# Performance work log

Measured on AMD Instinct MI355X. Metric: run time of the kernel, lower is better.

Reference implementation:

```python
import jax, jax.numpy as jnp
import numpy as np

G, N, E, F, D = 4096, 64, 256, 64, 128
H1, H2 = 16, 2
EP = 32768
EPS = 1e-15
MAX_LOGSTD = 10.0


def setup_inputs() -> dict:
    key = jax.random.key(0)
    ks = jax.random.split(key, 16)
    def lin(k, i, o):
        return (jax.random.normal(k, (i, o), jnp.float32) / np.sqrt(i)).astype(jnp.float32)
    inp = {}
    inp["x"] = jax.random.normal(ks[0], (G, N, F), jnp.float32)
    inp["edge_index"] = jax.random.randint(ks[1], (G, 2, E), 0, N, dtype=jnp.int32)
    inp["edge_weight"] = jax.random.uniform(ks[2], (G, E), jnp.float32)
    inp["pos_edges"] = jax.random.randint(ks[3], (2, EP), 0, G, dtype=jnp.int32)
    inp["neg_edges"] = jax.random.randint(ks[4], (2, EP), 0, G, dtype=jnp.int32)
    inp["eps"] = jax.random.normal(ks[5], (G, D), jnp.float32)
    inp["W_gcn1"] = lin(ks[6], F, D); inp["b_gcn1"] = jnp.zeros((D,), jnp.float32)
    inp["W_fc1"] = lin(ks[7], D, H1); inp["b_fc1"] = jnp.zeros((H1,), jnp.float32)
    inp["W_fc2"] = lin(ks[8], H1, H2); inp["b_fc2"] = jnp.zeros((H2,), jnp.float32)
    inp["W_c1"] = lin(ks[9], D, 2 * D); inp["b_c1"] = jnp.zeros((2 * D,), jnp.float32)
    inp["W_mu"] = lin(ks[10], 2 * D, D); inp["b_mu"] = jnp.zeros((D,), jnp.float32)
    inp["W_ls"] = lin(ks[11], 2 * D, D); inp["b_ls"] = jnp.zeros((D,), jnp.float32)
    inp["emb"] = jax.random.normal(ks[12], (G, D), jnp.float32)
    inp["W_lin1"] = lin(ks[13], 2 * D, 2 * D); inp["b_lin1"] = jnp.zeros((2 * D,), jnp.float32)
    inp["W_lin2"] = lin(ks[14], 2 * D, 2 * D); inp["b_lin2"] = jnp.zeros((2 * D,), jnp.float32)
    return inp


def gcn_conv(x, src, dst, w, W, b, n):
    # PyG GCNConv: add self-loops (weight 1), sym-normalize, aggregate at target (col).
    xw = x @ W                                      # [n, out]
    deg = jnp.zeros((n,), xw.dtype).at[dst].add(w) + 1.0
    dinv = jax.lax.rsqrt(deg)
    norm = dinv[src] * w * dinv[dst]
    agg = jnp.zeros_like(xw).at[dst].add(xw[src] * norm[:, None])
    agg = agg + xw * (dinv * dinv)[:, None]         # self-loop term
    return agg + b


def sage_graph(x, ei, w, W_gcn1, b_gcn1, W_fc1, b_fc1, W_fc2, b_fc2):
    src, dst = ei[0], ei[1]
    h = gcn_conv(x, src, dst, w, W_gcn1, b_gcn1, N)          # [N, D]
    a1 = jnp.tanh(h @ W_fc1 + b_fc1)                         # [N, H1]
    S = jax.nn.softmax(a1 @ W_fc2 + b_fc2, axis=1)           # [N, 2]
    # get_laplacian(normalization='sym'): L = I - D^{-1/2} A D^{-1/2}, deg from row
    deg = jnp.zeros((N,), x.dtype).at[src].add(w)
    dinv = jnp.where(deg > 0, jax.lax.rsqrt(jnp.maximum(deg, 1e-30)), 0.0)
    lw = -dinv[src] * w * dinv[dst]
    L = jnp.zeros((N, N), x.dtype).at[src, dst].add(lw) + jnp.eye(N, dtype=x.dtype)
    new_adj = S.T @ (L @ S)                                  # [2, 2]
    norm_adj = new_adj / jnp.maximum(jnp.sum(jnp.abs(new_adj), axis=1, keepdims=True), 1e-12)
    diag = jnp.diagonal(norm_adj)
    pos_penalty = jnp.mean((diag - 1.0) ** 2)                # MSE vs ones(2)
    g_emb = jnp.mean(S.T @ h, axis=0)                        # [D]
    return g_emb, pos_penalty


def gcn_conv_unw(x, src, dst, W, b, n):
    return gcn_conv(x, src, dst, jnp.ones(src.shape, x.dtype), W, b, n)


def reference(x, edge_index, edge_weight, pos_edges, neg_edges, eps,
              W_gcn1, b_gcn1, W_fc1, b_fc1, W_fc2, b_fc2,
              W_c1, b_c1, W_mu, b_mu, W_ls, b_ls, emb,
              W_lin1, b_lin1, W_lin2, b_lin2):
    g_embs, pens = jax.vmap(sage_graph,
                            in_axes=(0, 0, 0, None, None, None, None, None, None))(
        x, edge_index, edge_weight, W_gcn1, b_gcn1, W_fc1, b_fc1, W_fc2, b_fc2)
    positive_penalty = jnp.mean(pens)
    # VGAE encode over graph-level graph (dropout in eval mode = identity)
    ps, pd = pos_edges[0], pos_edges[1]
    h = jax.nn.relu(gcn_conv_unw(g_embs, ps, pd, W_c1, b_c1, G))
    mu = gcn_conv_unw(h, ps, pd, W_mu, b_mu, G)
    logstd = jnp.minimum(gcn_conv_unw(h, ps, pd, W_ls, b_ls, G), MAX_LOGSTD)
    z = mu + eps * jnp.exp(logstd)                            # reparametrize
    zc = jnp.concatenate([emb, z], axis=-1)                   # [G, 2D]
    def pred(ei):
        fx = zc[ei[0]] @ W_lin1 + b_lin1
        fy = zc[ei[1]] @ W_lin2 + b_lin2
        return jax.nn.sigmoid(jnp.sum(fx * fy, axis=1))
    pos_pred = pred(pos_edges)
    neg_pred = pred(neg_edges)
    rec_loss = -jnp.mean(jnp.log(pos_pred + EPS)) - jnp.mean(jnp.log(1.0 - neg_pred + EPS))
    kl = -0.5 * jnp.mean(jnp.sum(1.0 + 2.0 * logstd - mu ** 2 - jnp.exp(2.0 * logstd), axis=1))
    pre_loss = rec_loss + kl / G
    return pre_loss, positive_penalty, pos_pred, neg_pred
```

## Files before the change

### kernel.cpp

```cpp
#include <hip/hip_runtime.h>
#include <hip/hip_bf16.h>
#include <math.h>

#define GG   4096
#define NNODE 64
#define EEDGE 256
#define FFEAT 64
#define DDIM 128
#define EP   32768

__device__ __forceinline__ float fast_tanh(float x) {
    float e = __expf(2.0f * x);
    return 1.0f - 2.0f / (e + 1.0f);
}

__global__ void k_prep(const float* __restrict__ Wg, const float* __restrict__ Wf1,
                       const float* __restrict__ bf1, const float* __restrict__ bg,
                       float* __restrict__ Wgf1, float* __restrict__ bcomb,
                       float* __restrict__ bg32, int* __restrict__ icnt_g) {
    int t = threadIdx.x;
    for (int o = t; o < 1024; o += 256) {
        int r = o >> 4, j = o & 15;
        int kk = r >> 2, q = r & 3;
        int f = q * 16 + kk;
        float s = 0.f;
        for (int d = 0; d < 128; ++d) s += Wg[f * 128 + d] * Wf1[d * 16 + j];
        Wgf1[o] = s;
    }
    if (t < 16) {
        float s = bf1[t];
        for (int d = 0; d < 128; ++d) s += bg[d] * Wf1[d * 16 + t];
        bcomb[t] = s;
    }
    if (t >= 128) bg32[t - 128] = 32.0f * bg[t - 128];
    for (int i = t; i < 4096; i += 256) icnt_g[i] = 0;
}

__global__ __launch_bounds__(256) void k_pg(
    const float* __restrict__ x, const int* __restrict__ ei, const float* __restrict__ ew,
    const float* __restrict__ Wgf1, const float* __restrict__ bcomb,
    const float* __restrict__ Wf2, const float* __restrict__ bf2,
    float* __restrict__ Qh, float* __restrict__ pens)
{
    __shared__ __align__(16) float sm[6656];
    float* xs    = sm;
    float* Wp    = sm + 4352;
    int*   lsrc  = (int*)(sm + 5376);
    float* lnrm  = sm + 5632;
    int*   icnt  = (int*)(sm + 5888);
    int*   offs  = (int*)(sm + 5952);
    int*   curs  = (int*)(sm + 6016);
    float* degw  = sm + 6080;
    float* dinvs = sm + 6144;
    float* deg2s = sm + 6208;
    float* dinv2s= sm + 6272;
    float* Ss    = sm + 6336;
    float* LSs   = sm + 6464;
    float* bcs   = sm + 6592;
    float* Wf2s  = sm + 6608;
    float* bf2s  = sm + 6640;

    const int g = blockIdx.x;
    const int t = threadIdx.x;
    const float* xg = x + (size_t)g * 4096;

    int es, ed; float wv;
    {
        const int* eg = ei + (size_t)g * 512;
        es = eg[t];
        ed = eg[256 + t];
        wv = ew[(size_t)g * 256 + t];
        for (int i = t; i < 1024; i += 256) {
            int n = i >> 4, k = (i & 15) * 4;
            *(float4*)&xs[n * 68 + k] = *(const float4*)&xg[n * 64 + k];
        }
        *(float4*)&Wp[t * 4] = *(const float4*)&Wgf1[t * 4];
        if (t < 16) bcs[t] = bcomb[t];
        if (t < 32) Wf2s[t] = Wf2[t];
        if (t < 2)  bf2s[t] = bf2[t];
        if (t < 64) { icnt[t] = 0; degw[t] = 1.0f; deg2s[t] = 0.0f; }
        if (t < 128) LSs[t] = 0.0f;
    }
    __syncthreads();

    atomicAdd(&icnt[ed], 1);
    atomicAdd(&degw[ed], wv);
    atomicAdd(&deg2s[es], wv);
    __syncthreads();

    if (t < 64) {
        int v = icnt[t], own = v;
        for (int o = 1; o < 64; o <<= 1) { int u = __shfl_up(v, o); if (t >= o) v += u; }
        int excl = v - own;
        offs[t] = excl; curs[t] = excl;
        dinvs[t] = rsqrtf(degw[t]);
        float dg = deg2s[t];
        dinv2s[t] = dg > 0.0f ? rsqrtf(fmaxf(dg, 1e-30f)) : 0.0f;
    }
    __syncthreads();

    float lw;
    {
        int pos = atomicAdd(&curs[ed], 1);
        lsrc[pos] = es;
        lnrm[pos] = dinvs[es] * wv * dinvs[ed];
        lw = -dinv2s[es] * wv * dinv2s[ed];
    }
    __syncthreads();

    const int n = t >> 2, q = t & 3, base = q * 16;
    float Av[16];
    {
        float sc = dinvs[n] * dinvs[n];
        const float* xrow = &xs[n * 68 + base];
        *(float4*)&Av[0]  = *(const float4*)&xrow[0];
        *(float4*)&Av[4]  = *(const float4*)&xrow[4];
        *(float4*)&Av[8]  = *(const float4*)&xrow[8];
        *(float4*)&Av[12] = *(const float4*)&xrow[12];
#pragma unroll
        for (int kk = 0; kk < 16; ++kk) Av[kk] *= sc;
        int o = offs[n], c = icnt[n];
        for (int j = 0; j < c; ++j) {
            int s = lsrc[o + j];
            float nm = lnrm[o + j];
            const float* xr = &xs[s * 68 + base];
            float4 X0 = *(const float4*)&xr[0];
            float4 X1 = *(const float4*)&xr[4];
            float4 X2 = *(const float4*)&xr[8];
            float4 X3 = *(const float4*)&xr[12];
            Av[0]  += X0.x * nm; Av[1]  += X0.y * nm; Av[2]  += X0.z * nm; Av[3]  += X0.w * nm;
            Av[4]  += X1.x * nm; Av[5]  += X1.y * nm; Av[6]  += X1.z * nm; Av[7]  += X1.w * nm;
            Av[8]  += X2.x * nm; Av[9]  += X2.y * nm; Av[10] += X2.z * nm; Av[11] += X2.w * nm;
            Av[12] += X3.x * nm; Av[13] += X3.y * nm; Av[14] += X3.z * nm; Av[15] += X3.w * nm;
        }
        __syncthreads();
        float* xw = &xs[n * 68 + base];
        *(float4*)&xw[0]  = *(float4*)&Av[0];
        *(float4*)&xw[4]  = *(float4*)&Av[4];
        *(float4*)&xw[8]  = *(float4*)&Av[8];
        *(float4*)&xw[12] = *(float4*)&Av[12];
    }
    __syncthreads();

    {
        float pj[16];
#pragma unroll
        for (int j = 0; j < 16; ++j) pj[j] = 0.f;
#pragma unroll
        for (int kk = 0; kk < 16; ++kk) {
            float a = Av[kk];
            const float* wr = &Wp[((kk << 2) + q) << 4];
            float4 w0 = *(const float4*)&wr[0];
            float4 w1 = *(const float4*)&wr[4];
            float4 w2 = *(const float4*)&wr[8];
            float4 w3 = *(const float4*)&wr[12];
            pj[0]  += a * w0.x; pj[1]  += a * w0.y; pj[2]  += a * w0.z; pj[3]  += a * w0.w;
            pj[4]  += a * w1.x; pj[5]  += a * w1.y; pj[6]  += a * w1.z; pj[7]  += a * w1.w;
            pj[8]  += a * w2.x; pj[9]  += a * w2.y; pj[10] += a * w2.z; pj[11] += a * w2.w;
            pj[12] += a * w3.x; pj[13] += a * w3.y; pj[14] += a * w3.z; pj[15] += a * w3.w;
        }
#pragma unroll
        for (int j = 0; j < 16; ++j) {
            pj[j] += __shfl_xor(pj[j], 1);
            pj[j] += __shfl_xor(pj[j], 2);
        }
        float z0 = bf2s[0], z1 = bf2s[1];
#pragma unroll
        for (int j = 0; j < 16; ++j) {
            float aj = fast_tanh(pj[j] + bcs[j]);
            z0 += aj * Wf2s[2 * j];
            z1 += aj * Wf2s[2 * j + 1];
        }
        float m = fmaxf(z0, z1);
        float e0 = __expf(z0 - m), e1 = __expf(z1 - m);
        float inv = 1.0f / (e0 + e1);
        if (q == 0) { Ss[n * 2] = e0 * inv; Ss[n * 2 + 1] = e1 * inv; }
    }
    __syncthreads();

    {
        float s0 = Ss[ed * 2], s1 = Ss[ed * 2 + 1];
        atomicAdd(&LSs[es * 2],     lw * s0);
        atomicAdd(&LSs[es * 2 + 1], lw * s1);
    }
    __syncthreads();

    if (t < 64) {
        float s0 = Ss[t * 2], s1 = Ss[t * 2 + 1];
        float l0 = s0 + LSs[t * 2], l1 = s1 + LSs[t * 2 + 1];
        float p00 = s0 * l0, p01 = s0 * l1, p10 = s1 * l0, p11 = s1 * l1;
        for (int o = 32; o; o >>= 1) {
            p00 += __shfl_down(p00, o); p01 += __shfl_down(p01, o);
            p10 += __shfl_down(p10, o); p11 += __shfl_down(p11, o);
        }
        if (t == 0) {
            float r0 = fmaxf(fabsf(p00) + fabsf(p01), 1e-12f);
            float r1 = fmaxf(fabsf(p10) + fabsf(p11), 1e-12f);
            float d0 = p00 / r0 - 1.0f, d1 = p11 / r1 - 1.0f;
            pens[g] = 0.5f * (d0 * d0 + d1 * d1);
        }
    }
    {
        int k = t & 63, p = t >> 6;
        float qk = 0.f;
#pragma unroll 4
        for (int nn = 0; nn < 16; ++nn)
            qk += xs[(p * 16 + nn) * 68 + k];
        Wp[p * 64 + k] = qk;
    }
    __syncthreads();
    if (t < 64)
        Qh[(size_t)g * 64 + t] = 0.5f * (Wp[t] + Wp[64 + t] + Wp[128 + t] + Wp[192 + t]);
}

__global__ void k_cnt(const int* __restrict__ pd, int* __restrict__ icnt) {
    int e = blockIdx.x * 256 + threadIdx.x;
    atomicAdd(&icnt[pd[e]], 1);
}

__global__ void k_scan(const int* __restrict__ icnt, int* __restrict__ offs,
                       int* __restrict__ curs, float* __restrict__ dinv) {
    __shared__ int wsum[4];
    int t = threadIdx.x;
    int base = t * 16;
    int l0,l1,l2,l3,l4,l5,l6,l7,l8,l9,l10,l11,l12,l13,l14,l15;
    l0=icnt[base+0]; l1=icnt[base+1]; l2=icnt[base+2]; l3=icnt[base+3];
    l4=icnt[base+4]; l5=icnt[base+5]; l6=icnt[base+6]; l7=icnt[base+7];
    l8=icnt[base+8]; l9=icnt[base+9]; l10=icnt[base+10]; l11=icnt[base+11];
    l12=icnt[base+12]; l13=icnt[base+13]; l14=icnt[base+14]; l15=icnt[base+15];
    int s = l0+l1+l2+l3+l4+l5+l6+l7+l8+l9+l10+l11+l12+l13+l14+l15;
    int lane = t & 63, w = t >> 6;
    int v = s;
    for (int o = 1; o < 64; o <<= 1) { int u = __shfl_up(v, o); if (lane >= o) v += u; }
    if (lane == 63) wsum[w] = v;
    __syncthreads();
    int woff = 0;
    for (int i = 0; i < 4; ++i) if (i < w) woff += wsum[i];
    int run = woff + v - s;
#define SC(L, I) offs[base+(I)] = run; curs[base+(I)] = run; \
    dinv[base+(I)] = rsqrtf((float)(L) + 1.0f); run += L;
    SC(l0,0) SC(l1,1) SC(l2,2) SC(l3,3) SC(l4,4) SC(l5,5) SC(l6,6) SC(l7,7)
    SC(l8,8) SC(l9,9) SC(l10,10) SC(l11,11) SC(l12,12) SC(l13,13) SC(l14,14) SC(l15,15)
#undef SC
}

__global__ void k_place(const int* __restrict__ pe, const float* __restrict__ dinv,
                        int* __restrict__ curs, int* __restrict__ csr_src,
                        float* __restrict__ csr_nrm) {
    int e = blockIdx.x * 256 + threadIdx.x;
    int s = pe[e], d = pe[EP + e];
    int pos = atomicAdd(&curs[d], 1);
    csr_src[pos] = s;
    csr_nrm[pos] = dinv[s] * dinv[d];
}

__global__ void k_gather128(const int* __restrict__ offs, const int* __restrict__ icnt,
                            const int* __restrict__ csr_src, const float* __restrict__ csr_nrm,
                            const float* __restrict__ dinv, const float* __restrict__ in,
                            float* __restrict__ out) {
    int g = blockIdx.x, d = threadIdx.x;
    float dv = dinv[g];
    float acc = in[(size_t)g * 128 + d] * dv * dv;
    int o = offs[g], c = icnt[g];
    for (int j = 0; j < c; ++j)
        acc += in[(size_t)csr_src[o + j] * 128 + d] * csr_nrm[o + j];
    out[(size_t)g * 128 + d] = acc;
}

__global__ void k_gather256(const int* __restrict__ offs, const int* __restrict__ icnt,
                            const int* __restrict__ csr_src, const float* __restrict__ csr_nrm,
                            const float* __restrict__ dinv, const float* __restrict__ in,
                            float* __restrict__ out) {
    int g = blockIdx.x, d = threadIdx.x;
    float dv = dinv[g];
    float acc = in[(size_t)g * 256 + d] * dv * dv;
    int o = offs[g], c = icnt[g];
    for (int j = 0; j < c; ++j)
        acc += in[(size_t)csr_src[o + j] * 256 + d] * csr_nrm[o + j];
    out[(size_t)g * 256 + d] = acc;
}

__global__ __launch_bounds__(256) void k_gemm(
    const float* __restrict__ A,
    const float* __restrict__ B0, const float* __restrict__ bias0, float* __restrict__ C0,
    const float* __restrict__ B1, const float* __restrict__ bias1, float* __restrict__ C1,
    int M, int K, int N, int dorelu)
{
    __shared__ __align__(16) float lds[2 * 4352];
    const float* B = B0; const float* bias = bias0; float* C = C0;
    int by = blockIdx.y;
    if (B1 != nullptr && by >= (int)(gridDim.y >> 1)) {
        B = B1; bias = bias1; C = C1; by -= (gridDim.y >> 1);
    }
    const int mb = blockIdx.x * 64, nbb = by * 64;
    const int t = threadIdx.x;
    const int tm4 = (t >> 4) * 4, tn4 = (t & 15) * 4;
    const int ma = t >> 2, ka = (t & 3) * 8;
    const int kb = t >> 3, nb8 = (t & 7) * 8;

    float4 pa0, pa1, pb0, pb1;
#define LOADT(K0) { \
    const float* Ap = &A[(size_t)(mb + ma) * K + (K0) + ka]; \
    pa0 = *(const float4*)Ap; pa1 = *(const float4*)(Ap + 4); \
    const float* Bp = &B[(size_t)((K0) + kb) * N + nbb + nb8]; \
    pb0 = *(const float4*)Bp; pb1 = *(const float4*)(Bp + 4); }
#define STORET(BUF) { \
    float* At_ = lds + (BUF) * 4352; \
    At_[(ka + 0) * 68 + ma] = pa0.x; At_[(ka + 1) * 68 + ma] = pa0.y; \
    At_[(ka + 2) * 68 + ma] = pa0.z; At_[(ka + 3) * 68 + ma] = pa0.w; \
    At_[(ka + 4) * 68 + ma] = pa1.x; At_[(ka + 5) * 68 + ma] = pa1.y; \
    At_[(ka + 6) * 68 + ma] = pa1.z; At_[(ka + 7) * 68 + ma] = pa1.w; \
    float* Bs_ = lds + (BUF) * 4352 + 2176; \
    *(float4*)&Bs_[kb * 68 + nb8] = pb0; *(float4*)&Bs_[kb * 68 + nb8 + 4] = pb1; }

    float4 ca0 = {0,0,0,0}, ca1 = {0,0,0,0}, ca2 = {0,0,0,0}, ca3 = {0,0,0,0};
    const int nk0 = K >> 5;
    LOADT(0)
    STORET(0)
    __syncthreads();
    for (int it = 0; it < nk0; ++it) {
        if (it + 1 < nk0) LOADT((it + 1) * 32)
        const float* At_ = lds + (it & 1) * 4352;
        const float* Bs_ = At_ + 2176;
#pragma unroll
        for (int k = 0; k < 32; ++k) {
            float4 av = *(const float4*)&At_[k * 68 + tm4];
            float4 bv = *(const float4*)&Bs_[k * 68 + tn4];
            ca0.x += av.x * bv.x; ca0.y += av.x * bv.y; ca0.z += av.x * bv.z; ca0.w += av.x * bv.w;
            ca1.x += av.y * bv.x; ca1.y += av.y * bv.y; ca1.z += av.y * bv.z; ca1.w += av.y * bv.w;
            ca2.x += av.z * bv.x; ca2.y += av.z * bv.y; ca2.z += av.z * bv.z; ca2.w += av.z * bv.w;
            ca3.x += av.w * bv.x; ca3.y += av.w * bv.y; ca3.z += av.w * bv.z; ca3.w += av.w * bv.w;
        }
        if (it + 1 < nk0) {
            STORET((it + 1) & 1)
            __syncthreads();
        }
    }
#undef LOADT
#undef STORET
    float4 bv4 = {0, 0, 0, 0};
    if (bias) bv4 = *(const float4*)&bias[nbb + tn4];
#define CST(I, CV) { \
    float4 v; v.x = CV.x + bv4.x; v.y = CV.y + bv4.y; v.z = CV.z + bv4.z; v.w = CV.w + bv4.w; \
    if (dorelu) { v.x = fmaxf(v.x, 0.f); v.y = fmaxf(v.y, 0.f); v.z = fmaxf(v.z, 0.f); v.w = fmaxf(v.w, 0.f); } \
    *(float4*)&C[(size_t)(mb + tm4 + (I)) * N + nbb + tn4] = v; }
    CST(0, ca0) CST(1, ca1) CST(2, ca2) CST(3, ca3)
#undef CST
}

__global__ void k_fin_z(const float* __restrict__ mu_arr, const float* __restrict__ ls_arr,
                        const float* __restrict__ eps, const float* __restrict__ emb,
                        float* __restrict__ zc, float* __restrict__ klp) {
    __shared__ float smw[2];
    int g = blockIdx.x, d = threadIdx.x;
    int idx = g * 128 + d;
    float mu = mu_arr[idx];
    float ls = fminf(ls_arr[idx], 10.0f);
    float e  = __expf(ls);
    float z = mu + eps[idx] * e;
    zc[(size_t)g * 256 + d] = emb[idx];
    zc[(size_t)g * 256 + 128 + d] = z;
    float term = 1.0f + 2.0f * ls - mu * mu - e * e;
    for (int o = 32; o; o >>= 1) term += __shfl_down(term, o);
    if ((d & 63) == 0) smw[d >> 6] = term;
    __syncthreads();
    if (d == 0) klp[g] = smw[0] + smw[1];
}

__global__ void k_pred(const float* __restrict__ A, const float* __restrict__ B,
                       const int* __restrict__ pos, const int* __restrict__ neg,
                       float* __restrict__ out, float* __restrict__ predp) {
    __shared__ float smw[16];
    int t = threadIdx.x, sub = t >> 4, l = t & 15;
    int eg = blockIdx.x * 16 + sub;
    int isneg = eg >= EP;
    int e = eg - (isneg ? EP : 0);
    const int* eix = isneg ? neg : pos;
    int s = eix[e], d = eix[EP + e];
    const float4* Ar = (const float4*)(A + (size_t)s * 256);
    const float4* Br = (const float4*)(B + (size_t)d * 256);
    float dot = 0.f;
#pragma unroll
    for (int q = 0; q < 4; ++q) {
        float4 av = Ar[l + 16 * q], bv = Br[l + 16 * q];
        dot += av.x * bv.x + av.y * bv.y + av.z * bv.z + av.w * bv.w;
    }
    for (int o = 8; o; o >>= 1) dot += __shfl_down(dot, o);
    if (l == 0) {
        float p = 1.0f / (1.0f + __expf(-dot));
        float term;
        if (isneg) { out[2 + EP + e] = p; term = __logf(1.0f - p + 1e-15f); }
        else       { out[2 + e] = p;      term = __logf(p + 1e-15f); }
        smw[sub] = term;
    }
    __syncthreads();
    if (t == 0) {
        float s16 = 0.f;
#pragma unroll
        for (int i = 0; i < 16; ++i) s16 += smw[i];
        predp[blockIdx.x] = s16;
    }
}

__global__ void k_final(const float* __restrict__ pens, const float* __restrict__ klp,
                        const float* __restrict__ predp, float* __restrict__ out) {
    __shared__ float sm[16];
    int t = threadIdx.x;
    float s_pen = 0.f, s_kl = 0.f, s_pos = 0.f, s_neg = 0.f;
    for (int i = t; i < 4096; i += 256) { s_pen += pens[i]; s_kl += klp[i]; }
    for (int i = t; i < 2048; i += 256) { s_pos += predp[i]; s_neg += predp[2048 + i]; }
    for (int o = 32; o; o >>= 1) {
        s_pen += __shfl_down(s_pen, o); s_kl += __shfl_down(s_kl, o);
        s_pos += __shfl_down(s_pos, o); s_neg += __shfl_down(s_neg, o);
    }
    int w = t >> 6;
    if ((t & 63) == 0) { sm[w] = s_pen; sm[4 + w] = s_kl; sm[8 + w] = s_pos; sm[12 + w] = s_neg; }
    __syncthreads();
    if (t == 0) {
        float pen = sm[0] + sm[1] + sm[2] + sm[3];
        float kls = sm[4] + sm[5] + sm[6] + sm[7];
        float pos = sm[8] + sm[9] + sm[10] + sm[11];
        float neg = sm[12] + sm[13] + sm[14] + sm[15];
        float rec = -(pos / 32768.0f) - (neg / 32768.0f);
        out[0] = rec - 0.5f * kls / (4096.0f * 4096.0f);
        out[1] = pen * (1.0f / 4096.0f);
    }
}

extern "C" void kernel_launch(void* const* d_in, const int* in_sizes, int n_in,
                              void* d_out, int out_size, void* d_ws, size_t ws_size,
                              hipStream_t stream) {
    const float* x   = (const float*)d_in[0];
    const int*   ei  = (const int*)d_in[1];
    const float* ew  = (const float*)d_in[2];
    const int*   pos = (const int*)d_in[3];
    const int*   neg = (const int*)d_in[4];
    const float* eps = (const float*)d_in[5];
    const float* Wg  = (const float*)d_in[6];
    const float* bg  = (const float*)d_in[7];
    const float* Wf1 = (const float*)d_in[8];
    const float* bf1 = (const float*)d_in[9];
    const float* Wf2 = (const float*)d_in[10];
    const float* bf2 = (const float*)d_in[11];
    const float* Wc1 = (const float*)d_in[12];
    const float* bc1 = (const float*)d_in[13];
    const float* Wmu = (const float*)d_in[14];
    const float* bmu = (const float*)d_in[15];
    const float* Wls = (const float*)d_in[16];
    const float* bls = (const float*)d_in[17];
    const float* emb = (const float*)d_in[18];
    const float* Wl1 = (const float*)d_in[19];
    const float* bl1 = (const float*)d_in[20];
    const float* Wl2 = (const float*)d_in[21];
    const float* bl2 = (const float*)d_in[22];
    float* out = (float*)d_out;
    float* ws  = (float*)d_ws;

    float* g_embs  = ws + 0;
    float* dinv    = ws + 524288;
    int*   icnt_g  = (int*)(ws + 528384);
    int*   off_g   = (int*)(ws + 532480);
    int*   cur_g   = (int*)(ws + 536576);
    int*   csr_src = (int*)(ws + 540672);
    float* csr_nrm = ws + 573440;
    float* Qh      = ws + 606208;
    float* ga      = ws + 868352;
    float* h       = ws + 1392640;
    float* ha      = ws + 2441216;
    float* mu_arr  = ws + 3489792;
    float* ls_arr  = ws + 4014080;
    float* zc      = ws + 4538368;
    float* Abuf    = ws + 5586944;
    float* Bbuf    = ws + 6635520;
    float* pens    = ws + 7684096;
    float* klp     = ws + 7688192;
    float* predp   = ws + 7692288;
    float* Wgf1    = ws + 7708672;
    float* bcomb   = ws + 7709696;
    float* bg32    = ws + 7709712;

    k_prep<<<1, 256, 0, stream>>>(Wg, Wf1, bf1, bg, Wgf1, bcomb, bg32, icnt_g);
    k_pg<<<GG, 256, 0, stream>>>(x, ei, ew, Wgf1, bcomb, Wf2, bf2, Qh, pens);
    k_gemm<<<dim3(64, 2), 256, 0, stream>>>(Qh, Wg, bg32, g_embs,
                                            nullptr, nullptr, nullptr, GG, 64, 128, 0);

    k_cnt<<<EP / 256, 256, 0, stream>>>(pos + EP, icnt_g);
    k_scan<<<1, 256, 0, stream>>>(icnt_g, off_g, cur_g, dinv);
    k_place<<<EP / 256, 256, 0, stream>>>(pos, dinv, cur_g, csr_src, csr_nrm);

    k_gather128<<<GG, 128, 0, stream>>>(off_g, icnt_g, csr_src, csr_nrm, dinv, g_embs, ga);
    k_gemm<<<dim3(64, 4), 256, 0, stream>>>(ga, Wc1, bc1, h,
                                            nullptr, nullptr, nullptr, GG, 128, 256, 1);

    k_gather256<<<GG, 256, 0, stream>>>(off_g, icnt_g, csr_src, csr_nrm, dinv, h, ha);
    k_gemm<<<dim3(64, 4), 256, 0, stream>>>(ha, Wmu, bmu, mu_arr,
                                            Wls, bls, ls_arr, GG, 256, 128, 0);
    k_fin_z<<<GG, 128, 0, stream>>>(mu_arr, ls_arr, eps, emb, zc, klp);

    k_gemm<<<dim3(64, 8), 256, 0, stream>>>(zc, Wl1, bl1, Abuf,
                                            Wl2, bl2, Bbuf, GG, 256, 256, 0);

    k_pred<<<(2 * EP) / 16, 256, 0, stream>>>(Abuf, Bbuf, pos, neg, out, predp);
    k_final<<<1, 256, 0, stream>>>(pens, klp, predp, out);
}
```

Before: 320.8 us.

## Project node features before aggregation and compute pooled readout via column weights

Adds a separate kernel that multiplies all node features by the fused GCN-FC1 weight first, so per-graph aggregation works on 16-wide projected rows instead of 64-wide raw features. The per-graph kernel now uses much less shared memory. It computes the pooled readout Qh as a weighted sum of x rows, using per-node column sums of the normalization accumulated with atomics. The cost is an extra launch and a round trip of the projected features through global memory, plus re-reading x from global in the readout.

After: 337.9 us. 5.3% more time.

```diff
diff --git a/kernel.cpp b/kernel.cpp
--- a/kernel.cpp
+++ b/kernel.cpp
@@ -20,9 +20,7 @@
                        float* __restrict__ bg32, int* __restrict__ icnt_g) {
     int t = threadIdx.x;
     for (int o = t; o < 1024; o += 256) {
-        int r = o >> 4, j = o & 15;
-        int kk = r >> 2, q = r & 3;
-        int f = q * 16 + kk;
+        int f = o >> 4, j = o & 15;
         float s = 0.f;
         for (int d = 0; d < 128; ++d) s += Wg[f * 128 + d] * Wf1[d * 16 + j];
         Wgf1[o] = s;
@@ -36,33 +34,69 @@
     for (int i = t; i < 4096; i += 256) icnt_g[i] = 0;
 }
 
+__global__ __launch_bounds__(256) void k_y(
+    const float* __restrict__ x, const float* __restrict__ W,
+    float* __restrict__ Y)
+{
+    __shared__ __align__(16) float Ws[1024];
+    const int t = threadIdx.x;
+    *(float4*)&Ws[t * 4] = *(const float4*)&W[t * 4];
+    const int rr = t >> 2, q = t & 3;
+    const size_t r0 = (size_t)blockIdx.x * 256 + rr;
+    const float* x0 = &x[r0 * 64];
+    __syncthreads();
+    float4 p0 = {0,0,0,0}, p1 = {0,0,0,0}, p2 = {0,0,0,0}, p3 = {0,0,0,0};
+#pragma unroll 4
+    for (int kb = 0; kb < 16; ++kb) {
+        float4 xv0 = *(const float4*)&x0[kb * 4];
+        float4 xv1 = *(const float4*)&x0[4096 + kb * 4];
+        float4 xv2 = *(const float4*)&x0[8192 + kb * 4];
+        float4 xv3 = *(const float4*)&x0[12288 + kb * 4];
+#pragma unroll
+        for (int kk = 0; kk < 4; ++kk) {
+            float4 wv = *(const float4*)&Ws[(kb * 4 + kk) * 16 + q * 4];
+            float a0 = (&xv0.x)[kk], a1 = (&xv1.x)[kk];
+            float a2 = (&xv2.x)[kk], a3 = (&xv3.x)[kk];
+            p0.x += a0 * wv.x; p0.y += a0 * wv.y; p0.z += a0 * wv.z; p0.w += a0 * wv.w;
+            p1.x += a1 * wv.x; p1.y += a1 * wv.y; p1.z += a1 * wv.z; p1.w += a1 * wv.w;
+            p2.x += a2 * wv.x; p2.y += a2 * wv.y; p2.z += a2 * wv.z; p2.w += a2 * wv.w;
+            p3.x += a3 * wv.x; p3.y += a3 * wv.y; p3.z += a3 * wv.z; p3.w += a3 * wv.w;
+        }
+    }
+    float* y0 = &Y[r0 * 16 + q * 4];
+    *(float4*)&y0[0]          = p0;
+    *(float4*)&y0[64 * 16]    = p1;
+    *(float4*)&y0[128 * 16]   = p2;
+    *(float4*)&y0[192 * 16]   = p3;
+}
+
 __global__ __launch_bounds__(256) void k_pg(
-    const float* __restrict__ x, const int* __restrict__ ei, const float* __restrict__ ew,
-    const float* __restrict__ Wgf1, const float* __restrict__ bcomb,
+    const float* __restrict__ Yg, const int* __restrict__ ei, const float* __restrict__ ew,
+    const float* __restrict__ x, const float* __restrict__ bcomb,
     const float* __restrict__ Wf2, const float* __restrict__ bf2,
     float* __restrict__ Qh, float* __restrict__ pens)
 {
-    __shared__ __align__(16) float sm[6656];
-    float* xs    = sm;
-    float* Wp    = sm + 4352;
-    int*   lsrc  = (int*)(sm + 5376);
-    float* lnrm  = sm + 5632;
-    int*   icnt  = (int*)(sm + 5888);
-    int*   offs  = (int*)(sm + 5952);
-    int*   curs  = (int*)(sm + 6016);
-    float* degw  = sm + 6080;
-    float* dinvs = sm + 6144;
-    float* deg2s = sm + 6208;
-    float* dinv2s= sm + 6272;
-    float* Ss    = sm + 6336;
-    float* LSs   = sm + 6464;
-    float* bcs   = sm + 6592;
-    float* Wf2s  = sm + 6608;
-    float* bf2s  = sm + 6640;
+    __shared__ __align__(16) float sm[2624];
+    float* Ys    = sm;
+    int*   lsrc  = (int*)(sm + 1280);
+    float* lnrm  = sm + 1536;
+    int*   icnt  = (int*)(sm + 1792);
+    int*   offs  = (int*)(sm + 1856);
+    int*   curs  = (int*)(sm + 1920);
+    float* degw  = sm + 1984;
+    float* dinvs = sm + 2048;
+    float* deg2s = sm + 2112;
+    float* dinv2s= sm + 2176;
+    float* cws   = sm + 2240;
+    float* Ss    = sm + 2304;
+    float* LSs   = sm + 2432;
+    float* bcs   = sm + 2560;
+    float* Wf2s  = sm + 2576;
+    float* bf2s  = sm + 2608;
 
     const int g = blockIdx.x;
     const int t = threadIdx.x;
-    const float* xg = x + (size_t)g * 4096;
+    const int n = t >> 2, q = t & 3;
 
     int es, ed; float wv;
     {
@@ -70,11 +104,7 @@
         es = eg[t];
         ed = eg[256 + t];
         wv = ew[(size_t)g * 256 + t];
-        for (int i = t; i < 1024; i += 256) {
-            int n = i >> 4, k = (i & 15) * 4;
-            *(float4*)&xs[n * 68 + k] = *(const float4*)&xg[n * 64 + k];
-        }
-        *(float4*)&Wp[t * 4] = *(const float4*)&Wgf1[t * 4];
+        *(float4*)&Ys[n * 20 + q * 4] = *(const float4*)&Yg[(size_t)g * 1024 + t * 4];
         if (t < 16) bcs[t] = bcomb[t];
         if (t < 32) Wf2s[t] = Wf2[t];
         if (t < 2)  bf2s[t] = bf2[t];
@@ -93,7 +123,9 @@
         for (int o = 1; o < 64; o <<= 1) { int u = __shfl_up(v, o); if (t >= o) v += u; }
         int excl = v - own;
         offs[t] = excl; curs[t] = excl;
-        dinvs[t] = rsqrtf(degw[t]);
+        float dv = rsqrtf(degw[t]);
+        dinvs[t] = dv;
+        cws[t] = dv * dv;
         float dg = deg2s[t];
         dinv2s[t] = dg > 0.0f ? rsqrtf(fmaxf(dg, 1e-30f)) : 0.0f;
     }
@@ -102,79 +134,45 @@
     float lw;
     {
         int pos = atomicAdd(&curs[ed], 1);
+        float nm = dinvs[es] * wv * dinvs[ed];
         lsrc[pos] = es;
-        lnrm[pos] = dinvs[es] * wv * dinvs[ed];
+        lnrm[pos] = nm;
+        atomicAdd(&cws[es], nm);
         lw = -dinv2s[es] * wv * dinv2s[ed];
     }
     __syncthreads();
 
-    const int n = t >> 2, q = t & 3, base = q * 16;
-    float Av[16];
     {
-        float sc = dinvs[n] * dinvs[n];
-        const float* xrow = &xs[n * 68 + base];
-        *(float4*)&Av[0]  = *(const float4*)&xrow[0];
-        *(float4*)&Av[4]  = *(const float4*)&xrow[4];
-        *(float4*)&Av[8]  = *(const float4*)&xrow[8];
-        *(float4*)&Av[12] = *(const float4*)&xrow[12];
-#pragma unroll
-        for (int kk = 0; kk < 16; ++kk) Av[kk] *= sc;
+        float dv = dinvs[n];
+        float sc = dv * dv;
+        float4 acc = *(const float4*)&Ys[n * 20 + q * 4];
+        acc.x *= sc; acc.y *= sc; acc.z *= sc; acc.w *= sc;
         int o = offs[n], c = icnt[n];
         for (int j = 0; j < c; ++j) {
             int s = lsrc[o + j];
             float nm = lnrm[o + j];
-            const float* xr = &xs[s * 68 + base];
-            float4 X0 = *(const float4*)&xr[0];
-            float4 X1 = *(const float4*)&xr[4];
-            float4 X2 = *(const float4*)&xr[8];
-            float4 X3 = *(const float4*)&xr[12];
-            Av[0]  += X0.x * nm; Av[1]  += X0.y * nm; Av[2]  += X0.z * nm; Av[3]  += X0.w * nm;
-            Av[4]  += X1.x * nm; Av[5]  += X1.y * nm; Av[6]  += X1.z * nm; Av[7]  += X1.w * nm;
-            Av[8]  += X2.x * nm; Av[9]  += X2.y * nm; Av[10] += X2.z * nm; Av[11] += X2.w * nm;
-            Av[12] += X3.x * nm; Av[13] += X3.y * nm; Av[14] += X3.z * nm; Av[15] += X3.w * nm;
-        }
-        __syncthreads();
-        float* xw = &xs[n * 68 + base];
-        *(float4*)&xw[0]  = *(float4*)&Av[0];
-        *(float4*)&xw[4]  = *(float4*)&Av[4];
-        *(float4*)&xw[8]  = *(float4*)&Av[8];
-        *(float4*)&xw[12] = *(float4*)&Av[12];
-    }
-    __syncthreads();
-
-    {
-        float pj[16];
-#pragma unroll
-        for (int j = 0; j < 16; ++j) pj[j] = 0.f;
-#pragma unroll
-        for (int kk = 0; kk < 16; ++kk) {
-            float a = Av[kk];
-            const float* wr = &Wp[((kk << 2) + q) << 4];
-            float4 w0 = *(const float4*)&wr[0];
-            float4 w1 = *(const float4*)&wr[4];
-            float4 w2 = *(const float4*)&wr[8];
-            float4 w3 = *(const float4*)&wr[12];
-            pj[0]  += a * w0.x; pj[1]  += a * w0.y; pj[2]  += a * w0.z; pj[3]  += a * w0.w;
-            pj[4]  += a * w1.x; pj[5]  += a * w1.y; pj[6]  += a * w1.z; pj[7]  += a * w1.w;
-            pj[8]  += a * w2.x; pj[9]  += a * w2.y; pj[10] += a * w2.z; pj[11] += a * w2.w;
-            pj[12] += a * w3.x; pj[13] += a * w3.y; pj[14] += a * w3.z; pj[15] += a * w3.w;
-        }
-#pragma unroll
-        for (int j = 0; j < 16; ++j) {
-            pj[j] += __shfl_xor(pj[j], 1);
-            pj[j] += __shfl_xor(pj[j], 2);
-        }
-        float z0 = bf2s[0], z1 = bf2s[1];
-#pragma unroll
-        for (int j = 0; j < 16; ++j) {
-            float aj = fast_tanh(pj[j] + bcs[j]);
-            z0 += aj * Wf2s[2 * j];
-            z1 += aj * Wf2s[2 * j + 1];
-        }
-        float m = fmaxf(z0, z1);
-        float e0 = __expf(z0 - m), e1 = __expf(z1 - m);
-        float inv = 1.0f / (e0 + e1);
-        if (q == 0) { Ss[n * 2] = e0 * inv; Ss[n * 2 + 1] = e1 * inv; }
+            float4 yv = *(const float4*)&Ys[s * 20 + q * 4];
+            acc.x += yv.x * nm; acc.y += yv.y * nm;
+            acc.z += yv.z * nm; acc.w += yv.w * nm;
+        }
+        float4 bc4 = *(const float4*)&bcs[q * 4];
+        float t0 = fast_tanh(acc.x + bc4.x);
+        float t1 = fast_tanh(acc.y + bc4.y);
+        float t2 = fast_tanh(acc.z + bc4.z);
+        float t3 = fast_tanh(acc.w + bc4.w);
+        float4 wf0 = *(const float4*)&Wf2s[8 * q];
+        float4 wf1 = *(const float4*)&Wf2s[8 * q + 4];
+        float z0 = t0 * wf0.x + t1 * wf0.z + t2 * wf1.x + t3 * wf1.z;
+        float z1 = t0 * wf0.y + t1 * wf0.w + t2 * wf1.y + t3 * wf1.w;
+        z0 += __shfl_xor(z0, 1); z0 += __shfl_xor(z0, 2);
+        z1 += __shfl_xor(z1, 1); z1 += __shfl_xor(z1, 2);
+        if (q == 0) {
+            z0 += bf2s[0]; z1 += bf2s[1];
+            float m = fmaxf(z0, z1);
+            float e0 = __expf(z0 - m), e1 = __expf(z1 - m);
+            float inv = 1.0f / (e0 + e1);
+            Ss[n * 2] = e0 * inv; Ss[n * 2 + 1] = e1 * inv;
+        }
     }
     __syncthreads();
 
@@ -202,15 +200,17 @@
     }
     {
         int k = t & 63, p = t >> 6;
+        const float* xg = x + (size_t)g * 4096 + k;
         float qk = 0.f;
 #pragma unroll 4
-        for (int nn = 0; nn < 16; ++nn)
-            qk += xs[(p * 16 + nn) * 68 + k];
-        Wp[p * 64 + k] = qk;
+        for (int nn = p * 16; nn < p * 16 + 16; ++nn)
+            qk += cws[nn] * xg[(size_t)nn * 64];
+        __syncthreads();
+        Ys[p * 64 + k] = qk;
     }
     __syncthreads();
     if (t < 64)
-        Qh[(size_t)g * 64 + t] = 0.5f * (Wp[t] + Wp[64 + t] + Wp[128 + t] + Wp[192 + t]);
+        Qh[(size_t)g * 64 + t] = 0.5f * (Ys[t] + Ys[64 + t] + Ys[128 + t] + Ys[192 + t]);
 }
 
 __global__ void k_cnt(const int* __restrict__ pd, int* __restrict__ icnt) {
@@ -478,9 +478,11 @@
     float* Wgf1    = ws + 7708672;
     float* bcomb   = ws + 7709696;
     float* bg32    = ws + 7709712;
+    float* Y       = ws + 1392640;
 
     k_prep<<<1, 256, 0, stream>>>(Wg, Wf1, bf1, bg, Wgf1, bcomb, bg32, icnt_g);
-    k_pg<<<GG, 256, 0, stream>>>(x, ei, ew, Wgf1, bcomb, Wf2, bf2, Qh, pens);
+    k_y<<<1024, 256, 0, stream>>>(x, Wgf1, Y);
+    k_pg<<<GG, 256, 0, stream>>>(Y, ei, ew, x, bcomb, Wf2, bf2, Qh, pens);
     k_gemm<<<dim3(64, 2), 256, 0, stream>>>(Qh, Wg, bg32, g_embs,
                                             nullptr, nullptr, nullptr, GG, 64, 128, 0);
 
```
